# Kernel tuning notes

Measured on AMD Instinct MI355X. Metric: run time of the kernel, lower is better.

## Reference

```python
import jax, jax.numpy as jnp
import numpy as np

K = 16          # neighbors per node
EPS = 1e-5      # BatchNorm eps
BN_SCALE = 1.0 / np.sqrt(1.0 + EPS)  # eval BN with running mean=0, var=1


def _knn_idx(x, k):
    # x: [B, N, d] -> idx [B, N, k] of k nearest neighbors (self excluded)
    sq = jnp.sum(x * x, axis=-1)                               # [B, N]
    d2 = sq[:, :, None] + sq[:, None, :] - 2.0 * jnp.einsum('bnd,bmd->bnm', x, x)
    n = x.shape[1]
    d2 = jnp.where(jnp.eye(n, dtype=bool)[None], jnp.inf, d2)  # no self loops
    _, idx = jax.lax.top_k(-d2, k)
    return idx


def _edge_conv(x, idx, W, b, g, be):
    # PyG EdgeConv: max_j MLP([x_i, x_j - x_i]); MLP = Linear+BN(eval)+ReLU
    xj = jax.vmap(lambda xb, ib: xb[ib])(x, idx)               # [B, N, k, d]
    xi = x[:, :, None, :]
    m = jnp.concatenate([jnp.broadcast_to(xi, xj.shape), xj - xi], axis=-1)
    h = m @ W + b                                              # [B, N, k, out]
    h = g * (h * BN_SCALE) + be                                # eval BatchNorm
    h = jax.nn.relu(h)
    return jnp.max(h, axis=2)                                  # scatter-max over k


def setup_inputs() -> dict:
    key = jax.random.key(0)
    ks = jax.random.split(key, 16)
    B, N, D, C = 128, 256, 6, 12

    def w(k_, shape, fan_in):
        return (jax.random.normal(k_, shape, jnp.float32) / np.sqrt(fan_in)).astype(jnp.float32)

    inp = {
        'x':   jax.random.normal(ks[0], (B, N, D), jnp.float32),
        'W1':  w(ks[1], (2 * 6, 64), 12),   'b1': jnp.zeros((64,), jnp.float32),
        'g1':  jnp.ones((64,), jnp.float32), 'be1': jnp.zeros((64,), jnp.float32),
        'W2':  w(ks[2], (2 * 64, 128), 128), 'b2': jnp.zeros((128,), jnp.float32),
        'g2':  jnp.ones((128,), jnp.float32), 'be2': jnp.zeros((128,), jnp.float32),
        'W3':  w(ks[3], (2 * 128, 256), 256), 'b3': jnp.zeros((256,), jnp.float32),
        'g3':  jnp.ones((256,), jnp.float32), 'be3': jnp.zeros((256,), jnp.float32),
        'Wf1': w(ks[4], (256, 128), 256),    'bf1': jnp.zeros((128,), jnp.float32),
        'gf':  jnp.ones((128,), jnp.float32), 'bef': jnp.zeros((128,), jnp.float32),
        'Wf2': w(ks[5], (128, C), 128),      'bf2': jnp.zeros((C,), jnp.float32),
    }
    return inp


def reference(x, W1, b1, g1, be1, W2, b2, g2, be2, W3, b3, g3, be3,
              Wf1, bf1, gf, bef, Wf2, bf2):
    h = _edge_conv(x, _knn_idx(x, K), W1, b1, g1, be1)   # [B, N, 64]
    h = _edge_conv(h, _knn_idx(h, K), W2, b2, g2, be2)   # [B, N, 128]
    h = _edge_conv(h, _knn_idx(h, K), W3, b3, g3, be3)   # [B, N, 256]
    p = jnp.max(h, axis=1)                               # global_max_pool [B, 256]
    f = jax.nn.relu(gf * ((p @ Wf1 + bf1) * BN_SCALE) + bef)
    return f @ Wf2 + bf2                                 # [B, num_classes]
```

## Files before the change

kernel.cpp:

```cpp
#include <hip/hip_runtime.h>
#include <cstdint>
#include <cstddef>

#define KNN 16
#define NPTS 256
#define NBATCH 128

static constexpr float BN_SCALE_F = 0.9999950000374997f;

__device__ inline unsigned int f32_ord(float f) {
    unsigned int u = __float_as_uint(f);
    return (u & 0x80000000u) ? ~u : (u | 0x80000000u);
}

__device__ __forceinline__ int wmap(int n) { return n + 4 * (n >> 4); }

template<int D>
__global__ __launch_bounds__(256) void sq_kernel(const float* __restrict__ x,
                                                 float* __restrict__ sq) {
    const int t = blockIdx.x * 256 + threadIdx.x;
    const float* r = x + (size_t)t * D;
    float s = 0.f;
    #pragma unroll
    for (int d = 0; d < D; ++d) s = fmaf(r[d], r[d], s);
    sq[t] = s;
}

template<int D>
__global__ __launch_bounds__(512) void knn_fused_kernel(
        const float* __restrict__ x, const float* __restrict__ sq,
        int* __restrict__ idx) {
    constexpr int KS = (D >= 16) ? 16 : D;
    constexpr int NSTEP = D / KS;
    constexpr int NLA = (128 * KS + 511) / 512;
    constexpr int NLB = (256 * KS + 511) / 512;
    const int t  = threadIdx.x;
    const int tx = t & 31, ty = t >> 5;
    const int sr = t >> 2, sch = t & 3;
    const int b  = blockIdx.x >> 1;
    const int i0 = (blockIdx.x & 1) * 128;
    const int base = b * NPTS;

    __shared__ float As[2][KS][132];
    __shared__ float Bs[2][KS][260];
    __shared__ float d2L[128][132];
    __shared__ unsigned char Mi[128][68];

    float4 pa, pb[2];
    float  pas[NLA], pbs[NLB];
    if constexpr (D % 16 == 0) {
        {
            const int r = t >> 2, cq = (t & 3) * 4;
            pa = *(const float4*)(x + (size_t)(base + i0 + r) * D + cq);
        }
        #pragma unroll
        for (int u = 0; u < 2; ++u) {
            const int e = t + u * 512, r = e >> 2, cq = (e & 3) * 4;
            pb[u] = *(const float4*)(x + (size_t)(base + r) * D + cq);
        }
    } else {
        #pragma unroll
        for (int u = 0; u < NLA; ++u) {
            const int e = t + u * 512;
            if (e < 128 * KS) {
                const int r = e / KS, c = e % KS;
                pas[u] = x[(size_t)(base + i0 + r) * D + c];
            }
        }
        #pragma unroll
        for (int u = 0; u < NLB; ++u) {
            const int e = t + u * 512;
            if (e < 256 * KS) {
                const int r = e / KS, c = e % KS;
                pbs[u] = x[(size_t)(base + r) * D + c];
            }
        }
    }

    float sqi[8];
    #pragma unroll
    for (int m = 0; m < 8; ++m) sqi[m] = sq[base + i0 + ty * 8 + m];

    float acc[8][8] = {};

    for (int s = 0; s < NSTEP; ++s) {
        const int buf = s & 1;
        if constexpr (D % 16 == 0) {
            {
                const int r = t >> 2, cq = (t & 3) * 4;
                As[buf][cq + 0][r] = pa.x; As[buf][cq + 1][r] = pa.y;
                As[buf][cq + 2][r] = pa.z; As[buf][cq + 3][r] = pa.w;
            }
            #pragma unroll
            for (int u = 0; u < 2; ++u) {
                const int e = t + u * 512, r = e >> 2, cq = (e & 3) * 4;
                Bs[buf][cq + 0][r] = pb[u].x; Bs[buf][cq + 1][r] = pb[u].y;
                Bs[buf][cq + 2][r] = pb[u].z; Bs[buf][cq + 3][r] = pb[u].w;
            }
        } else {
            #pragma unroll
            for (int u = 0; u < NLA; ++u) {
                const int e = t + u * 512;
                if (e < 128 * KS) {
                    const int r = e / KS, c = e % KS;
                    As[buf][c][r] = pas[u];
                }
            }
            #pragma unroll
            for (int u = 0; u < NLB; ++u) {
                const int e = t + u * 512;
                if (e < 256 * KS) {
                    const int r = e / KS, c = e % KS;
                    Bs[buf][c][r] = pbs[u];
                }
            }
        }

        __syncthreads();

        if (s + 1 < NSTEP) {
            const int k0n = (s + 1) * KS;
            if constexpr (D % 16 == 0) {
                {
                    const int r = t >> 2, cq = (t & 3) * 4;
                    pa = *(const float4*)(x + (size_t)(base + i0 + r) * D + k0n + cq);
                }
                #pragma unroll
                for (int u = 0; u < 2; ++u) {
                    const int e = t + u * 512, r = e >> 2, cq = (e & 3) * 4;
                    pb[u] = *(const float4*)(x + (size_t)(base + r) * D + k0n + cq);
                }
            } else {
                #pragma unroll
                for (int u = 0; u < NLA; ++u) {
                    const int e = t + u * 512;
                    if (e < 128 * KS) {
                        const int r = e / KS, c = e % KS;
                        pas[u] = x[(size_t)(base + i0 + r) * D + k0n + c];
                    }
                }
                #pragma unroll
                for (int u = 0; u < NLB; ++u) {
                    const int e = t + u * 512;
                    if (e < 256 * KS) {
                        const int r = e / KS, c = e % KS;
                        pbs[u] = x[(size_t)(base + r) * D + k0n + c];
                    }
                }
            }
        }

        #pragma unroll
        for (int kk = 0; kk < KS; ++kk) {
            float am[8], bm[8];
            *(float4*)&am[0] = *(const float4*)&As[buf][kk][ty * 8];
            *(float4*)&am[4] = *(const float4*)&As[buf][kk][ty * 8 + 4];
            #pragma unroll
            for (int n = 0; n < 8; ++n)
                bm[n] = Bs[buf][kk][n * 32 + tx];
            #pragma unroll
            for (int m = 0; m < 8; ++m)
                #pragma unroll
                for (int n = 0; n < 8; ++n)
                    acc[m][n] = fmaf(am[m], bm[n], acc[m][n]);
        }
    }

    unsigned int Lv[16], Li[16];
    #pragma unroll
    for (int q = 0; q < 16; ++q) { Lv[q] = 0xFFFFFFFFu; Li[q] = 0u; }

    __syncthreads();

    #pragma unroll
    for (int ph = 0; ph < 2; ++ph) {
        float sqj[4];
        #pragma unroll
        for (int n2 = 0; n2 < 4; ++n2)
            sqj[n2] = sq[base + ph * 128 + n2 * 32 + tx];
        #pragma unroll
        for (int m = 0; m < 8; ++m) {
            const int gi = i0 + ty * 8 + m;
            #pragma unroll
            for (int n2 = 0; n2 < 4; ++n2) {
                float v = (sqi[m] + sqj[n2]) - 2.f * acc[m][ph * 4 + n2];
                if (gi == ph * 128 + n2 * 32 + tx) v = INFINITY;
                d2L[ty * 8 + m][n2 * 32 + tx] = v;
            }
        }
        __syncthreads();

        #pragma unroll 4
        for (int i = 0; i < 32; ++i) {
            const unsigned int v = f32_ord(d2L[sr][sch + 4 * i]);
            const unsigned int j = (unsigned int)(ph * 128 + sch + 4 * i);
            #pragma unroll
            for (int q = 15; q >= 1; --q) {
                const bool a = v < Lv[q];
                const bool c = v < Lv[q - 1];
                Lv[q] = a ? (c ? Lv[q - 1] : v) : Lv[q];
                Li[q] = a ? (c ? Li[q - 1] : j) : Li[q];
            }
            const bool a0 = v < Lv[0];
            Lv[0] = a0 ? v : Lv[0];
            Li[0] = a0 ? j : Li[0];
        }
        __syncthreads();
    }

    #pragma unroll
    for (int q = 0; q < 16; ++q) {
        d2L[sr][sch * 16 + q] = __uint_as_float(Lv[q]);
        Mi[sr][sch * 16 + q]  = (unsigned char)Li[q];
    }
    __syncthreads();

    if (t < 128) {
        const int row = t;
        int h[4];
        unsigned int cv[4], ci[4];
        #pragma unroll
        for (int c = 0; c < 4; ++c) {
            h[c]  = 0;
            cv[c] = __float_as_uint(d2L[row][c * 16]);
            ci[c] = Mi[row][c * 16];
        }
        int outj[16];
        #pragma unroll
        for (int rd = 0; rd < 16; ++rd) {
            unsigned int bv = cv[0], bi = ci[0];
            int bc = 0;
            #pragma unroll
            for (int c = 1; c < 4; ++c) {
                const bool tk = (cv[c] < bv) | ((cv[c] == bv) & (ci[c] < bi));
                bv = tk ? cv[c] : bv;
                bi = tk ? ci[c] : bi;
                bc = tk ? c     : bc;
            }
            outj[rd] = (int)bi;
            #pragma unroll
            for (int c = 0; c < 4; ++c) {
                if (c == bc) {
                    const int hn = h[c] + 1;
                    h[c] = hn;
                    if (hn < 16) {
                        cv[c] = __float_as_uint(d2L[row][c * 16 + hn]);
                        ci[c] = Mi[row][c * 16 + hn];
                    } else {
                        cv[c] = 0xFFFFFFFFu;
                    }
                }
            }
        }
        int4* op = (int4*)(idx + (size_t)(base + i0 + row) * KNN);
        op[0] = make_int4(outj[0],  outj[1],  outj[2],  outj[3]);
        op[1] = make_int4(outj[4],  outj[5],  outj[6],  outj[7]);
        op[2] = make_int4(outj[8],  outj[9],  outj[10], outj[11]);
        op[3] = make_int4(outj[12], outj[13], outj[14], outj[15]);
    }
}

template<int D, int C>
__global__ __launch_bounds__(256) void mlp_gemm_kernel(
        const float* __restrict__ x, const float* __restrict__ W,
        const float* __restrict__ bias, const float* __restrict__ g,
        const float* __restrict__ be,
        float* __restrict__ A, float* __restrict__ Bv) {
    constexpr int BM = 128;
    constexpr int KT = (D >= 16) ? 16 : D;
    constexpr int NSTEP = D / KT;
    constexpr int NXG = (BM * KT + 255) / 256;
    constexpr int NWG = (KT * 128 + 255) / 256;
    const int t  = threadIdx.x;
    const int tx = t & 15;
    const int ty = t >> 4;
    const int m0 = blockIdx.x * BM;
    const int n0 = blockIdx.y * 128;

    __shared__ float Xs[2][KT][132];
    __shared__ float Ws[2][KT][164];

    float acc[8][8] = {};

    const int xr = t >> 1, xc = (t & 1) * 8;
    const int wk = t >> 4, nq = (t & 15) * 8;
    const int gn = n0 + nq;
    const bool isTop = (gn < C);
    const int wcol = isTop ? gn : (gn - C);
    const int mb = wmap(nq);

    float4 px0, px1;
    float4 wt0, wt1, wb0, wb1;
    float  pxg[NXG], pwg[NWG];

    if constexpr (D % 16 == 0) {
        const float* xp = x + (size_t)(m0 + xr) * D + xc;
        px0 = *(const float4*)(xp);
        px1 = *(const float4*)(xp + 4);
        const float* pT = W + (size_t)wk * C + wcol;
        const float* pB = W + (size_t)(D + wk) * C + wcol;
        wt0 = *(const float4*)(pT); wt1 = *(const float4*)(pT + 4);
        wb0 = *(const float4*)(pB); wb1 = *(const float4*)(pB + 4);
    } else {
        #pragma unroll
        for (int u = 0; u < NXG; ++u) {
            const int e = t + u * 256;
            if (e < BM * KT) {
                const int r = e / KT, c = e % KT;
                pxg[u] = x[(size_t)(m0 + r) * D + c];
            }
        }
        #pragma unroll
        for (int u = 0; u < NWG; ++u) {
            const int e = t + u * 256;
            if (e < KT * 128) {
                const int k = e >> 7, n = e & 127;
                const int g2 = n0 + n;
                pwg[u] = (g2 < C)
                    ? W[(size_t)k * C + g2] - W[(size_t)(D + k) * C + g2]
                    : W[(size_t)(D + k) * C + (g2 - C)];
            }
        }
    }

    for (int s = 0; s < NSTEP; ++s) {
        const int buf = s & 1;
        if constexpr (D % 16 == 0) {
            Xs[buf][xc + 0][xr] = px0.x; Xs[buf][xc + 1][xr] = px0.y;
            Xs[buf][xc + 2][xr] = px0.z; Xs[buf][xc + 3][xr] = px0.w;
            Xs[buf][xc + 4][xr] = px1.x; Xs[buf][xc + 5][xr] = px1.y;
            Xs[buf][xc + 6][xr] = px1.z; Xs[buf][xc + 7][xr] = px1.w;
            float4 v0, v1;
            if (isTop) {
                v0 = make_float4(wt0.x - wb0.x, wt0.y - wb0.y,
                                 wt0.z - wb0.z, wt0.w - wb0.w);
                v1 = make_float4(wt1.x - wb1.x, wt1.y - wb1.y,
                                 wt1.z - wb1.z, wt1.w - wb1.w);
            } else {
                v0 = wb0; v1 = wb1;
            }
            *(float4*)&Ws[buf][wk][mb]     = v0;
            *(float4*)&Ws[buf][wk][mb + 4] = v1;
        } else {
            #pragma unroll
            for (int u = 0; u < NXG; ++u) {
                const int e = t + u * 256;
                if (e < BM * KT) {
                    const int r = e / KT, c = e % KT;
                    Xs[buf][c][r] = pxg[u];
                }
            }
            #pragma unroll
            for (int u = 0; u < NWG; ++u) {
                const int e = t + u * 256;
                if (e < KT * 128) {
                    const int k = e >> 7, n = e & 127;
                    Ws[buf][k][wmap(n)] = pwg[u];
                }
            }
        }

        __syncthreads();

        if (s + 1 < NSTEP) {
            const int k0n = (s + 1) * KT;
            if constexpr (D % 16 == 0) {
                const float* xp = x + (size_t)(m0 + xr) * D + k0n + xc;
                px0 = *(const float4*)(xp);
                px1 = *(const float4*)(xp + 4);
                const float* pT = W + (size_t)(k0n + wk) * C + wcol;
                const float* pB = W + (size_t)(D + k0n + wk) * C + wcol;
                wt0 = *(const float4*)(pT); wt1 = *(const float4*)(pT + 4);
                wb0 = *(const float4*)(pB); wb1 = *(const float4*)(pB + 4);
            } else {
                #pragma unroll
                for (int u = 0; u < NXG; ++u) {
                    const int e = t + u * 256;
                    if (e < BM * KT) {
                        const int r = e / KT, c = e % KT;
                        pxg[u] = x[(size_t)(m0 + r) * D + k0n + c];
                    }
                }
                #pragma unroll
                for (int u = 0; u < NWG; ++u) {
                    const int e = t + u * 256;
                    if (e < KT * 128) {
                        const int k = e >> 7, n = e & 127;
                        const int g2 = n0 + n;
                        pwg[u] = (g2 < C)
                            ? W[(size_t)(k0n + k) * C + g2] - W[(size_t)(D + k0n + k) * C + g2]
                            : W[(size_t)(D + k0n + k) * C + (g2 - C)];
                    }
                }
            }
        }

        const int mc = wmap(tx * 8);
        #pragma unroll
        for (int kk = 0; kk < KT; ++kk) {
            float xm[8], wn[8];
            *(float4*)&xm[0] = *(const float4*)&Xs[buf][kk][ty * 8];
            *(float4*)&xm[4] = *(const float4*)&Xs[buf][kk][ty * 8 + 4];
            *(float4*)&wn[0] = *(const float4*)&Ws[buf][kk][mc];
            *(float4*)&wn[4] = *(const float4*)&Ws[buf][kk][mc + 4];
            #pragma unroll
            for (int m = 0; m < 8; ++m)
                #pragma unroll
                for (int n = 0; n < 8; ++n)
                    acc[m][n] = fmaf(xm[m], wn[n], acc[m][n]);
        }
    }

    if (isTop) {
        float fac[8];
        #pragma unroll
        for (int e = 0; e < 8; ++e) fac[e] = g[gn + e] * BN_SCALE_F;
        #pragma unroll
        for (int m = 0; m < 8; ++m) {
            float o[8];
            #pragma unroll
            for (int e = 0; e < 8; ++e) o[e] = fac[e] * acc[m][e];
            float* dst = A + (size_t)(m0 + ty * 8 + m) * C + gn;
            *(float4*)(dst)     = make_float4(o[0], o[1], o[2], o[3]);
            *(float4*)(dst + 4) = make_float4(o[4], o[5], o[6], o[7]);
        }
    } else {
        const int cb = gn - C;
        float fac[8], bb[8], bee[8];
        #pragma unroll
        for (int e = 0; e < 8; ++e) {
            fac[e] = g[cb + e] * BN_SCALE_F;
            bb[e]  = bias[cb + e];
            bee[e] = be[cb + e];
        }
        #pragma unroll
        for (int m = 0; m < 8; ++m) {
            float o[8];
            #pragma unroll
            for (int e = 0; e < 8; ++e)
                o[e] = fmaf(fac[e], acc[m][e] + bb[e], bee[e]);
            float* dst = Bv + (size_t)(m0 + ty * 8 + m) * C + cb;
            *(float4*)(dst)     = make_float4(o[0], o[1], o[2], o[3]);
            *(float4*)(dst + 4) = make_float4(o[4], o[5], o[6], o[7]);
        }
    }
}

template<int C>
__global__ __launch_bounds__(256) void combine_kernel(
        const float* A, const float* __restrict__ Bv,
        const int* __restrict__ idx, float* out) {
    constexpr int CQ = C / 4;
    constexpr int G  = 256 / CQ;
    const int tid = threadIdx.x;
    const int bi0 = blockIdx.x * G;
    __shared__ int nbr[G * KNN];
    if (tid < G * KNN) {
        const int p = tid >> 4, kk = tid & 15;
        nbr[p * KNN + kk] = idx[(size_t)(bi0 + p) * KNN + kk];
    }
    __syncthreads();
    const int p = tid / CQ;
    const int q = tid % CQ;
    const int gi = bi0 + p;
    const int b0 = gi & ~255;
    const float4* Bv4 = (const float4*)Bv;
    float4 mx = make_float4(-INFINITY, -INFINITY, -INFINITY, -INFINITY);
    #pragma unroll
    for (int kk = 0; kk < KNN; ++kk) {
        const int r = b0 + nbr[p * KNN + kk];
        const float4 v = Bv4[(size_t)r * CQ + q];
        mx.x = fmaxf(mx.x, v.x); mx.y = fmaxf(mx.y, v.y);
        mx.z = fmaxf(mx.z, v.z); mx.w = fmaxf(mx.w, v.w);
    }
    const float4 a = ((const float4*)A)[(size_t)gi * CQ + q];
    float4 o;
    o.x = fmaxf(a.x + mx.x, 0.f);
    o.y = fmaxf(a.y + mx.y, 0.f);
    o.z = fmaxf(a.z + mx.z, 0.f);
    o.w = fmaxf(a.w + mx.w, 0.f);
    ((float4*)out)[(size_t)gi * CQ + q] = o;
}

__global__ __launch_bounds__(256) void head_kernel(
        const float* __restrict__ h3, const float* __restrict__ Wf1,
        const float* __restrict__ bf1, const float* __restrict__ gf,
        const float* __restrict__ bef, const float* __restrict__ Wf2,
        const float* __restrict__ bf2, float* __restrict__ out) {
    const int b   = blockIdx.x;
    const int tid = threadIdx.x;
    __shared__ float p[256];
    __shared__ float f[128];
    const float* hb = h3 + (size_t)b * NPTS * 256;
    float mx = -INFINITY;
    for (int n = 0; n < NPTS; ++n) mx = fmaxf(mx, hb[(size_t)n * 256 + tid]);
    p[tid] = mx;
    __syncthreads();
    if (tid < 128) {
        float acc = bf1[tid];
        for (int d = 0; d < 256; ++d)
            acc = fmaf(p[d], Wf1[(size_t)d * 128 + tid], acc);
        float v = gf[tid] * (acc * BN_SCALE_F) + bef[tid];
        f[tid] = fmaxf(v, 0.f);
    }
    __syncthreads();
    if (tid < 12) {
        float acc = bf2[tid];
        for (int d = 0; d < 128; ++d)
            acc = fmaf(f[d], Wf2[(size_t)d * 12 + tid], acc);
        out[(size_t)b * 12 + tid] = acc;
    }
}

extern "C" void kernel_launch(void* const* d_in, const int* in_sizes, int n_in,
                              void* d_out, int out_size, void* d_ws, size_t ws_size,
                              hipStream_t stream) {
    const float* x   = (const float*)d_in[0];
    const float* W1  = (const float*)d_in[1];
    const float* b1  = (const float*)d_in[2];
    const float* g1  = (const float*)d_in[3];
    const float* be1 = (const float*)d_in[4];
    const float* W2  = (const float*)d_in[5];
    const float* b2  = (const float*)d_in[6];
    const float* g2  = (const float*)d_in[7];
    const float* be2 = (const float*)d_in[8];
    const float* W3  = (const float*)d_in[9];
    const float* b3  = (const float*)d_in[10];
    const float* g3  = (const float*)d_in[11];
    const float* be3 = (const float*)d_in[12];
    const float* Wf1 = (const float*)d_in[13];
    const float* bf1 = (const float*)d_in[14];
    const float* gf  = (const float*)d_in[15];
    const float* bef = (const float*)d_in[16];
    const float* Wf2 = (const float*)d_in[17];
    const float* bf2 = (const float*)d_in[18];
    float* out = (float*)d_out;

    char* ws = (char*)d_ws;
    const size_t idx_bytes = (size_t)NBATCH * NPTS * KNN * sizeof(int);
    const size_t reg_bytes = (size_t)NBATCH * NPTS * 256 * sizeof(float);
    int*   idx = (int*)ws;
    float* R1  = (float*)(ws + idx_bytes);
    float* R2  = (float*)(ws + idx_bytes + reg_bytes);
    float* R3  = (float*)(ws + idx_bytes + 2 * reg_bytes);
    float* sqb = (float*)(ws + idx_bytes + 3 * reg_bytes);

    const int BN = NBATCH * NPTS;
    const int KNN_GRID = NBATCH * 2;
    const int MB = BN / 128;

    sq_kernel<6><<<BN / 256, 256, 0, stream>>>(x, sqb);
    knn_fused_kernel<6><<<KNN_GRID, 512, 0, stream>>>(x, sqb, idx);
    mlp_gemm_kernel<6, 64><<<dim3(MB, 1), 256, 0, stream>>>(
        x, W1, b1, g1, be1, R1, R2);
    combine_kernel<64><<<BN / 16, 256, 0, stream>>>(R1, R2, idx, R1);

    sq_kernel<64><<<BN / 256, 256, 0, stream>>>(R1, sqb);
    knn_fused_kernel<64><<<KNN_GRID, 512, 0, stream>>>(R1, sqb, idx);
    mlp_gemm_kernel<64, 128><<<dim3(MB, 2), 256, 0, stream>>>(
        R1, W2, b2, g2, be2, R2, R3);
    combine_kernel<128><<<BN / 8, 256, 0, stream>>>(R2, R3, idx, R2);

    sq_kernel<128><<<BN / 256, 256, 0, stream>>>(R2, sqb);
    knn_fused_kernel<128><<<KNN_GRID, 512, 0, stream>>>(R2, sqb, idx);
    mlp_gemm_kernel<128, 256><<<dim3(MB, 4), 256, 0, stream>>>(
        R2, W3, b3, g3, be3, R3, R1);
    combine_kernel<256><<<BN / 4, 256, 0, stream>>>(R3, R1, idx, R3);

    head_kernel<<<NBATCH, 256, 0, stream>>>(R3, Wf1, bf1, gf, bef, Wf2, bf2, out);
}
```

Before: 437.9 us.

## Fuse squared-norm computation into kNN kernel and parallelize head pooling

The separate sq_kernel launches are removed. Each kNN block now computes the squared norms of its batch's 256 points into shared memory, which saves three launches and a global round trip. The tile-loop barrier is moved after the next-tile prefetch, and a redundant barrier before the distance write-out is dropped. The head kernel's global max pool is split across 1024 threads, each scanning a quarter of the points, followed by a shared-memory reduction, to shorten the serial per-thread load chain. The tradeoff is that the in-kernel norm loop reads rows with a per-thread stride, and the work is repeated by both half-blocks of each batch.

```diff
diff --git a/kernel.cpp b/kernel.cpp
--- a/kernel.cpp
+++ b/kernel.cpp
@@ -16,20 +16,8 @@
 __device__ __forceinline__ int wmap(int n) { return n + 4 * (n >> 4); }
 
 template<int D>
-__global__ __launch_bounds__(256) void sq_kernel(const float* __restrict__ x,
-                                                 float* __restrict__ sq) {
-    const int t = blockIdx.x * 256 + threadIdx.x;
-    const float* r = x + (size_t)t * D;
-    float s = 0.f;
-    #pragma unroll
-    for (int d = 0; d < D; ++d) s = fmaf(r[d], r[d], s);
-    sq[t] = s;
-}
-
-template<int D>
 __global__ __launch_bounds__(512) void knn_fused_kernel(
-        const float* __restrict__ x, const float* __restrict__ sq,
-        int* __restrict__ idx) {
+        const float* __restrict__ x, int* __restrict__ idx) {
     constexpr int KS = (D >= 16) ? 16 : D;
     constexpr int NSTEP = D / KS;
     constexpr int NLA = (128 * KS + 511) / 512;
@@ -45,6 +33,7 @@
     __shared__ float Bs[2][KS][260];
     __shared__ float d2L[128][132];
     __shared__ unsigned char Mi[128][68];
+    __shared__ float sqS[256];
 
     float4 pa, pb[2];
     float  pas[NLA], pbs[NLB];
@@ -77,9 +66,18 @@
         }
     }
 
+    if (t < 256) {
+        const float* r = x + (size_t)(base + t) * D;
+        float ssum = 0.f;
+        #pragma unroll
+        for (int d = 0; d < D; ++d) ssum = fmaf(r[d], r[d], ssum);
+        sqS[t] = ssum;
+    }
+    __syncthreads();
+
     float sqi[8];
     #pragma unroll
-    for (int m = 0; m < 8; ++m) sqi[m] = sq[base + i0 + ty * 8 + m];
+    for (int m = 0; m < 8; ++m) sqi[m] = sqS[i0 + ty * 8 + m];
 
     float acc[8][8] = {};
 
@@ -116,8 +114,6 @@
             }
         }
 
-        __syncthreads();
-
         if (s + 1 < NSTEP) {
             const int k0n = (s + 1) * KS;
             if constexpr (D % 16 == 0) {
@@ -150,6 +146,8 @@
             }
         }
 
+        __syncthreads();
+
         #pragma unroll
         for (int kk = 0; kk < KS; ++kk) {
             float am[8], bm[8];
@@ -170,14 +168,12 @@
     #pragma unroll
     for (int q = 0; q < 16; ++q) { Lv[q] = 0xFFFFFFFFu; Li[q] = 0u; }
 
-    __syncthreads();
-
     #pragma unroll
     for (int ph = 0; ph < 2; ++ph) {
         float sqj[4];
         #pragma unroll
         for (int n2 = 0; n2 < 4; ++n2)
-            sqj[n2] = sq[base + ph * 128 + n2 * 32 + tx];
+            sqj[n2] = sqS[ph * 128 + n2 * 32 + tx];
         #pragma unroll
         for (int m = 0; m < 8; ++m) {
             const int gi = i0 + ty * 8 + m;
@@ -482,19 +478,27 @@
     ((float4*)out)[(size_t)gi * CQ + q] = o;
 }
 
-__global__ __launch_bounds__(256) void head_kernel(
+__global__ __launch_bounds__(1024) void head_kernel(
         const float* __restrict__ h3, const float* __restrict__ Wf1,
         const float* __restrict__ bf1, const float* __restrict__ gf,
         const float* __restrict__ bef, const float* __restrict__ Wf2,
         const float* __restrict__ bf2, float* __restrict__ out) {
     const int b   = blockIdx.x;
     const int tid = threadIdx.x;
+    __shared__ float pp[4][256];
     __shared__ float p[256];
     __shared__ float f[128];
     const float* hb = h3 + (size_t)b * NPTS * 256;
+    const int c  = tid & 255;
+    const int q4 = tid >> 8;
     float mx = -INFINITY;
-    for (int n = 0; n < NPTS; ++n) mx = fmaxf(mx, hb[(size_t)n * 256 + tid]);
-    p[tid] = mx;
+    for (int n = q4 * 64; n < q4 * 64 + 64; ++n)
+        mx = fmaxf(mx, hb[(size_t)n * 256 + c]);
+    pp[q4][c] = mx;
+    __syncthreads();
+    if (tid < 256)
+        p[tid] = fmaxf(fmaxf(pp[0][tid], pp[1][tid]),
+                       fmaxf(pp[2][tid], pp[3][tid]));
     __syncthreads();
     if (tid < 128) {
         float acc = bf1[tid];
@@ -543,29 +547,25 @@
     float* R1  = (float*)(ws + idx_bytes);
     float* R2  = (float*)(ws + idx_bytes + reg_bytes);
     float* R3  = (float*)(ws + idx_bytes + 2 * reg_bytes);
-    float* sqb = (float*)(ws + idx_bytes + 3 * reg_bytes);
 
     const int BN = NBATCH * NPTS;
     const int KNN_GRID = NBATCH * 2;
     const int MB = BN / 128;
 
-    sq_kernel<6><<<BN / 256, 256, 0, stream>>>(x, sqb);
-    knn_fused_kernel<6><<<KNN_GRID, 512, 0, stream>>>(x, sqb, idx);
+    knn_fused_kernel<6><<<KNN_GRID, 512, 0, stream>>>(x, idx);
     mlp_gemm_kernel<6, 64><<<dim3(MB, 1), 256, 0, stream>>>(
         x, W1, b1, g1, be1, R1, R2);
     combine_kernel<64><<<BN / 16, 256, 0, stream>>>(R1, R2, idx, R1);
 
-    sq_kernel<64><<<BN / 256, 256, 0, stream>>>(R1, sqb);
-    knn_fused_kernel<64><<<KNN_GRID, 512, 0, stream>>>(R1, sqb, idx);
+    knn_fused_kernel<64><<<KNN_GRID, 512, 0, stream>>>(R1, idx);
     mlp_gemm_kernel<64, 128><<<dim3(MB, 2), 256, 0, stream>>>(
         R1, W2, b2, g2, be2, R2, R3);
     combine_kernel<128><<<BN / 8, 256, 0, stream>>>(R2, R3, idx, R2);
 
-    sq_kernel<128><<<BN / 256, 256, 0, stream>>>(R2, sqb);
-    knn_fused_kernel<128><<<KNN_GRID, 512, 0, stream>>>(R2, sqb, idx);
+    knn_fused_kernel<128><<<KNN_GRID, 512, 0, stream>>>(R2, idx);
     mlp_gemm_kernel<128, 256><<<dim3(MB, 4), 256, 0, stream>>>(
         R2, W3, b3, g3, be3, R3, R1);
     combine_kernel<256><<<BN / 4, 256, 0, stream>>>(R3, R1, idx, R3);
 
-    head_kernel<<<NBATCH, 256, 0, stream>>>(R3, Wf1, bf1, gf, bef, Wf2, bf2, out);
+    head_kernel<<<NBATCH, 1024, 0, stream>>>(R3, Wf1, bf1, gf, bef, Wf2, bf2, out);
 }
```

New measurement: 399.1 us (median of 2 runs). 1.1x faster.
